# Performance work log

Measured on AMD Instinct MI355X. Metric: run time of the kernel, lower is better.

Reference implementation:

```python
import jax, jax.numpy as jnp
import numpy as np

N_EMBD = 1024
HEAD_SIZE = 64
B, T = 4, 4096


def setup_inputs() -> dict:
    key = jax.random.key(0)
    kx, kq, kk, kv = jax.random.split(key, 4)
    x = jax.random.normal(kx, (B, T, N_EMBD), dtype=jnp.float32)
    Wq = jax.random.normal(kq, (N_EMBD, HEAD_SIZE), dtype=jnp.float32) * (N_EMBD ** -0.5)
    Wk = jax.random.normal(kk, (N_EMBD, HEAD_SIZE), dtype=jnp.float32) * (N_EMBD ** -0.5)
    Wv = jax.random.normal(kv, (N_EMBD, HEAD_SIZE), dtype=jnp.float32) * (N_EMBD ** -0.5)
    return {"x": x, "Wq": Wq, "Wk": Wk, "Wv": Wv}


def reference(x, Wq, Wk, Wv):
    # x: [B, T, C]; projections: [B, T, H]
    Bv, Tv, C = x.shape
    q = jnp.einsum('btc,ch->bth', x, Wq)
    k = jnp.einsum('btc,ch->bth', x, Wk)
    v = jnp.einsum('btc,ch->bth', x, Wv)
    # NOTE: original scales by C**-0.5 where C = n_embd (not head_size)
    scale = C ** -0.5
    wei = jnp.einsum('bth,bsh->bts', q, k) * scale  # [B, T, T]
    causal = jnp.tril(jnp.ones((Tv, Tv), dtype=bool))
    wei = jnp.where(causal[None, :, :], wei, -jnp.inf)
    wei = jax.nn.softmax(wei, axis=-1)
    # dropout p=0.0 (eval) -> identity
    out = jnp.einsum('bts,bsh->bth', wei, v)  # [B, T, H]
    return out
```

## Files before the change

### kernel.cpp

```cpp
#include <hip/hip_runtime.h>
#include <math.h>

#define Tt 4096
#define Cc 1024
#define Hh 64

typedef __attribute__((ext_vector_type(8))) short bf16x8;
typedef __attribute__((ext_vector_type(4))) float f32x4;
typedef unsigned int u32;

__device__ inline unsigned short f2bf(float f) {
    unsigned u = __float_as_uint(f);
    u = (u + 0x7FFFu + ((u >> 16) & 1u)) >> 16;
    return (unsigned short)u;
}

__global__ __launch_bounds__(256) void wt_build(
    const float* __restrict__ Wq, const float* __restrict__ Wk,
    const float* __restrict__ Wv, unsigned short* __restrict__ Wt)
{
    int e = blockIdx.x * 256 + threadIdx.x;
    int k = e & 1023, n = e >> 10;
    float v;
    if (n < 64)       v = Wq[k * 64 + n] * 0.03125f;
    else if (n < 128) v = Wk[k * 64 + (n - 64)];
    else              v = Wv[k * 64 + (n - 128)];
    Wt[n * 1024 + k] = f2bf(v);
}

__global__ __launch_bounds__(256, 2) void qkv_gemm(
    const float* __restrict__ x, const unsigned short* __restrict__ wt,
    unsigned short* __restrict__ qb, unsigned short* __restrict__ kb,
    unsigned short* __restrict__ vt)
{
    __shared__ unsigned short as_[32 * 1024];

    const int t = threadIdx.x, w = t >> 6, lane = t & 63;
    const int col = lane & 15, quad = lane >> 4;
    const int m0 = blockIdx.x * 32;

    {
        const float* xr = x + (long)m0 * Cc;
#pragma unroll
        for (int i = 0; i < 32; ++i) {
            float4 v = *(const float4*)&xr[i * Cc + t * 4];
            ushort4 pk = { f2bf(v.x), f2bf(v.y), f2bf(v.z), f2bf(v.w) };
            int woff = (t * 4) ^ ((i & 7) << 3);
            *(ushort4*)&as_[i * 1024 + woff] = pk;
        }
    }
    __syncthreads();

    const unsigned short* aB[2];
#pragma unroll
    for (int kc = 0; kc < 2; ++kc)
        aB[kc] = &as_[col * 1024 + ((kc * 32 + quad * 8) ^ ((col & 7) << 3))];

    const unsigned short* pB[3];
#pragma unroll
    for (int nt = 0; nt < 3; ++nt)
        pB[nt] = wt + ((w * 3 + nt) * 16 + col) * 1024 + quad * 8;

    f32x4 acc[2][3];
#pragma unroll
    for (int mt = 0; mt < 2; ++mt)
#pragma unroll
        for (int nt = 0; nt < 3; ++nt) acc[mt][nt] = (f32x4){0.f, 0.f, 0.f, 0.f};

    bf16x8 bfr[2][3][2];
    bf16x8 afr[2][2][2];

#pragma unroll
    for (int nt = 0; nt < 3; ++nt)
#pragma unroll
        for (int kc = 0; kc < 2; ++kc)
            bfr[0][nt][kc] = *(const bf16x8*)(pB[nt] + kc * 32);
#pragma unroll
    for (int mt = 0; mt < 2; ++mt)
#pragma unroll
        for (int kc = 0; kc < 2; ++kc)
            afr[0][mt][kc] = *(const bf16x8*)(aB[kc] + mt * 16 * 1024);

#pragma unroll
    for (int k = 0; k < 16; ++k) {
        const int cur = k & 1, nxt = cur ^ 1;
        if (k < 15) {
            const int ko = (k + 1) * 64;
#pragma unroll
            for (int nt = 0; nt < 3; ++nt)
#pragma unroll
                for (int kc = 0; kc < 2; ++kc)
                    bfr[nxt][nt][kc] = *(const bf16x8*)(pB[nt] + ko + kc * 32);
#pragma unroll
            for (int mt = 0; mt < 2; ++mt)
#pragma unroll
                for (int kc = 0; kc < 2; ++kc)
                    afr[nxt][mt][kc] = *(const bf16x8*)(aB[kc] + mt * 16 * 1024 + ko);
        }
#pragma unroll
        for (int kc = 0; kc < 2; ++kc)
#pragma unroll
            for (int nt = 0; nt < 3; ++nt)
#pragma unroll
                for (int mt = 0; mt < 2; ++mt)
                    acc[mt][nt] = __builtin_amdgcn_mfma_f32_16x16x32_bf16(
                        afr[cur][mt][kc], bfr[cur][nt][kc], acc[mt][nt], 0, 0, 0);
    }

    const long bidx = m0 >> 12;
    const int tbase = m0 & 4095;
#pragma unroll
    for (int mt = 0; mt < 2; ++mt)
#pragma unroll
        for (int nt = 0; nt < 3; ++nt) {
            int ntg = w * 3 + nt;
            int n = ntg * 16 + col;
            int row = m0 + mt * 16 + quad * 4;
            if (ntg < 4) {
#pragma unroll
                for (int reg = 0; reg < 4; ++reg)
                    qb[(long)(row + reg) * Hh + n] = f2bf(acc[mt][nt][reg]);
            } else if (ntg < 8) {
#pragma unroll
                for (int reg = 0; reg < 4; ++reg)
                    kb[(long)(row + reg) * Hh + (n - 64)] = f2bf(acc[mt][nt][reg]);
            } else {
                int h = n - 128;
                ushort4 pk = { f2bf(acc[mt][nt][0]), f2bf(acc[mt][nt][1]),
                               f2bf(acc[mt][nt][2]), f2bf(acc[mt][nt][3]) };
                *(ushort4*)&vt[(bidx * Hh + h) * (long)Tt + tbase + mt * 16 + quad * 4] = pk;
            }
        }
}

#define LDP 56
#define LDO 68

__global__ __launch_bounds__(256) void attn(
    const unsigned short* __restrict__ qg, const unsigned short* __restrict__ kg,
    const unsigned short* __restrict__ vtg,
    float* __restrict__ po, float* __restrict__ pls)
{
    __shared__ __align__(16) char smem[49664];
    float* o_red       = (float*)smem;
    float* lred        = (float*)(smem + 34816);
    unsigned short* pl = (unsigned short*)(smem + 35328);

    const int p    = blockIdx.x;
    const int qt   = 127 - (p >> 3);
    const int b    = p & 3;
    const int half = (p >> 2) & 1;
    const int tid  = (b << 7) | qt;
    const long qrow0 = (long)b * Tt + qt * 32;
    const int nkt = qt + 1;
    const int n0  = (nkt + 1) >> 1;
    const int cnt = half ? (nkt - n0) : n0;
    const int ust = half ? n0 : 0;

    const int t = threadIdx.x, w = t >> 6, lane = t & 63;
    const int col = lane & 15, quad = lane >> 4;
    const int plbase = w * 32 * LDP;

    bf16x8 qf[2][2];
#pragma unroll
    for (int mt = 0; mt < 2; ++mt)
#pragma unroll
        for (int kc = 0; kc < 2; ++kc)
            qf[mt][kc] = *(const bf16x8*)&qg[(qrow0 + mt * 16 + col) * Hh + kc * 32 + quad * 8];

    f32x4 oacc[2][4];
#pragma unroll
    for (int mt = 0; mt < 2; ++mt)
#pragma unroll
        for (int nt = 0; nt < 4; ++nt) oacc[mt][nt] = (f32x4){0.f, 0.f, 0.f, 0.f};
    float lsum[2][4] = {{0.f,0.f,0.f,0.f},{0.f,0.f,0.f,0.f}};

    for (int iu = w; iu < cnt; iu += 4) {
        const int u = ust + iu;
        const long krow0 = (long)b * Tt + u * 32;
        bf16x8 kf[2][2];
#pragma unroll
        for (int nt = 0; nt < 2; ++nt)
#pragma unroll
            for (int kc = 0; kc < 2; ++kc)
                kf[nt][kc] = *(const bf16x8*)&kg[(krow0 + nt * 16 + col) * Hh + kc * 32 + quad * 8];
        f32x4 s[2][2];
#pragma unroll
        for (int mt = 0; mt < 2; ++mt)
#pragma unroll
            for (int nt = 0; nt < 2; ++nt) {
                s[mt][nt] = (f32x4){0.f, 0.f, 0.f, 0.f};
#pragma unroll
                for (int kc = 0; kc < 2; ++kc)
                    s[mt][nt] = __builtin_amdgcn_mfma_f32_16x16x32_bf16(qf[mt][kc], kf[nt][kc], s[mt][nt], 0, 0, 0);
            }
#pragma unroll
        for (int mt = 0; mt < 2; ++mt)
#pragma unroll
            for (int reg = 0; reg < 4; ++reg) {
                int rloc = mt * 16 + quad * 4 + reg;
                if (u == qt) {
                    if (col > rloc)      s[mt][0][reg] = -INFINITY;
                    if (16 + col > rloc) s[mt][1][reg] = -INFINITY;
                }
                float p0 = __expf(s[mt][0][reg]);
                float p1 = __expf(s[mt][1][reg]);
                lsum[mt][reg] += p0 + p1;
                pl[plbase + rloc * LDP + col]      = f2bf(p0);
                pl[plbase + rloc * LDP + 16 + col] = f2bf(p1);
            }
        bf16x8 af0 = *(const bf16x8*)&pl[plbase + col * LDP + quad * 8];
        bf16x8 af1 = *(const bf16x8*)&pl[plbase + (16 + col) * LDP + quad * 8];
#pragma unroll
        for (int nt = 0; nt < 4; ++nt) {
            bf16x8 vf = *(const bf16x8*)&vtg[((long)b * Hh + nt * 16 + col) * Tt + u * 32 + quad * 8];
            oacc[0][nt] = __builtin_amdgcn_mfma_f32_16x16x32_bf16(af0, vf, oacc[0][nt], 0, 0, 0);
            oacc[1][nt] = __builtin_amdgcn_mfma_f32_16x16x32_bf16(af1, vf, oacc[1][nt], 0, 0, 0);
        }
    }

#pragma unroll
    for (int mt = 0; mt < 2; ++mt)
#pragma unroll
        for (int reg = 0; reg < 4; ++reg) {
            float l = lsum[mt][reg];
            l += __shfl_xor(l, 1); l += __shfl_xor(l, 2);
            l += __shfl_xor(l, 4); l += __shfl_xor(l, 8);
            if (col == 0) lred[w * 32 + mt * 16 + quad * 4 + reg] = l;
        }
#pragma unroll
    for (int mt = 0; mt < 2; ++mt)
#pragma unroll
        for (int nt = 0; nt < 4; ++nt)
#pragma unroll
            for (int reg = 0; reg < 4; ++reg)
                o_red[(w * 32 + mt * 16 + quad * 4 + reg) * LDO + nt * 16 + col] = oacc[mt][nt][reg];
    __syncthreads();
    if (t < 32)
        pls[(tid * 2 + half) * 32 + t] = lred[t] + lred[32 + t] + lred[64 + t] + lred[96 + t];
    float* pob = po + ((long)tid * 2 + half) * 2048;
#pragma unroll
    for (int j = 0; j < 8; ++j) {
        int e = t + 256 * j, r = e >> 6, c = e & 63;
        pob[e] = o_red[r * LDO + c] + o_red[(32 + r) * LDO + c]
               + o_red[(64 + r) * LDO + c] + o_red[(96 + r) * LDO + c];
    }
}

__global__ __launch_bounds__(256) void combine(
    const float* __restrict__ po, const float* __restrict__ pls, float* __restrict__ out)
{
    const int g = blockIdx.x;
    const long orow = (((long)(g >> 7)) * Tt + (long)(g & 127) * 32) * Hh;
    const float* p0 = po + (long)g * 2 * 2048;
    const float* p1 = p0 + 2048;
    const float* l0 = pls + g * 2 * 32;
    const float* l1 = l0 + 32;
    const int t = threadIdx.x;
#pragma unroll
    for (int j = 0; j < 8; ++j) {
        int e = t + 256 * j, r = e >> 6;
        out[orow + e] = (p0[e] + p1[e]) / (l0[r] + l1[r]);
    }
}

extern "C" void kernel_launch(void* const* d_in, const int* in_sizes, int n_in,
                              void* d_out, int out_size, void* d_ws, size_t ws_size,
                              hipStream_t stream)
{
    const float* x  = (const float*)d_in[0];
    const float* Wq = (const float*)d_in[1];
    const float* Wk = (const float*)d_in[2];
    const float* Wv = (const float*)d_in[3];
    float* outp = (float*)d_out;

    unsigned short* wt = (unsigned short*)d_ws;
    unsigned short* qb = wt + 196608;
    unsigned short* kb = qb + 1048576;
    unsigned short* vt = kb + 1048576;
    float* po  = (float*)(vt + 1048576);
    float* pls = po + 2097152;

    wt_build<<<dim3(768), dim3(256), 0, stream>>>(Wq, Wk, Wv, wt);
    qkv_gemm<<<dim3(512), dim3(256), 0, stream>>>(x, wt, qb, kb, vt);
    attn<<<dim3(1024), dim3(256), 0, stream>>>(qb, kb, vt, po, pls);
    combine<<<dim3(512), dim3(256), 0, stream>>>(po, pls, outp);
}
```

Measured before the change: 160.4 us.

## Pre-cast x to bf16 and stage GEMM tile via direct global-to-LDS loads

Adds a separate kernel that converts x from fp32 to bf16 in workspace. The QKV GEMM then fills its LDS tile with global_load_lds directly, keeping the same XOR swizzle. The attention kernel also aliases its P staging buffer onto the O-reduction buffer, which shrinks LDS use and may raise occupancy. The cost is an extra launch and an extra full read/write pass over x, plus a risk of a race from the aliased LDS if the reuse phases overlap.

```diff
diff --git a/kernel.cpp b/kernel.cpp
--- a/kernel.cpp
+++ b/kernel.cpp
@@ -13,6 +13,24 @@
     unsigned u = __float_as_uint(f);
     u = (u + 0x7FFFu + ((u >> 16) & 1u)) >> 16;
     return (unsigned short)u;
+}
+
+__device__ inline void gl_lds16(const unsigned short* g, unsigned short* l) {
+    __builtin_amdgcn_global_load_lds(
+        (const __attribute__((address_space(1))) u32*)g,
+        (__attribute__((address_space(3))) u32*)l, 16, 0, 0);
+}
+
+__global__ __launch_bounds__(256) void xcast(
+    const float* __restrict__ x, unsigned short* __restrict__ xb)
+{
+    const long i = ((long)blockIdx.x * 256 + threadIdx.x) * 8;
+    float4 a = *(const float4*)&x[i];
+    float4 b = *(const float4*)&x[i + 4];
+    ushort4 lo = { f2bf(a.x), f2bf(a.y), f2bf(a.z), f2bf(a.w) };
+    ushort4 hi = { f2bf(b.x), f2bf(b.y), f2bf(b.z), f2bf(b.w) };
+    *(ushort4*)&xb[i]     = lo;
+    *(ushort4*)&xb[i + 4] = hi;
 }
 
 __global__ __launch_bounds__(256) void wt_build(
@@ -29,7 +47,7 @@
 }
 
 __global__ __launch_bounds__(256, 2) void qkv_gemm(
-    const float* __restrict__ x, const unsigned short* __restrict__ wt,
+    const unsigned short* __restrict__ xbf, const unsigned short* __restrict__ wt,
     unsigned short* __restrict__ qb, unsigned short* __restrict__ kb,
     unsigned short* __restrict__ vt)
 {
@@ -40,13 +58,14 @@
     const int m0 = blockIdx.x * 32;
 
     {
-        const float* xr = x + (long)m0 * Cc;
-#pragma unroll
-        for (int i = 0; i < 32; ++i) {
-            float4 v = *(const float4*)&xr[i * Cc + t * 4];
-            ushort4 pk = { f2bf(v.x), f2bf(v.y), f2bf(v.z), f2bf(v.w) };
-            int woff = (t * 4) ^ ((i & 7) << 3);
-            *(ushort4*)&as_[i * 1024 + woff] = pk;
+        const int rh = t >> 7;
+        const int s  = t & 127;
+        const unsigned short* src = xbf + (long)m0 * 1024;
+#pragma unroll
+        for (int j = 0; j < 16; ++j) {
+            int r = 2 * j + rh;
+            gl_lds16(src + r * 1024 + (s ^ (r & 7)) * 8,
+                     as_ + j * 2048 + w * 512);
         }
     }
     __syncthreads();
@@ -141,10 +160,10 @@
     const unsigned short* __restrict__ vtg,
     float* __restrict__ po, float* __restrict__ pls)
 {
-    __shared__ __align__(16) char smem[49664];
+    __shared__ __align__(16) char smem[35328];
     float* o_red       = (float*)smem;
     float* lred        = (float*)(smem + 34816);
-    unsigned short* pl = (unsigned short*)(smem + 35328);
+    unsigned short* pl = (unsigned short*)smem;
 
     const int p    = blockIdx.x;
     const int qt   = 127 - (p >> 3);
@@ -159,7 +178,7 @@
 
     const int t = threadIdx.x, w = t >> 6, lane = t & 63;
     const int col = lane & 15, quad = lane >> 4;
-    const int plbase = w * 32 * LDP;
+    const int plbase = w * 4352;
 
     bf16x8 qf[2][2];
 #pragma unroll
@@ -280,9 +299,11 @@
     unsigned short* vt = kb + 1048576;
     float* po  = (float*)(vt + 1048576);
     float* pls = po + 2097152;
-
-    wt_build<<<dim3(768), dim3(256), 0, stream>>>(Wq, Wk, Wv, wt);
-    qkv_gemm<<<dim3(512), dim3(256), 0, stream>>>(x, wt, qb, kb, vt);
-    attn<<<dim3(1024), dim3(256), 0, stream>>>(qb, kb, vt, po, pls);
-    combine<<<dim3(512), dim3(256), 0, stream>>>(po, pls, outp);
-}
+    unsigned short* xbf = (unsigned short*)(pls + 32768);
+
+    xcast   <<<dim3(8192), dim3(256), 0, stream>>>(x, xbf);
+    wt_build<<<dim3(768),  dim3(256), 0, stream>>>(Wq, Wk, Wv, wt);
+    qkv_gemm<<<dim3(512),  dim3(256), 0, stream>>>(xbf, wt, qb, kb, vt);
+    attn    <<<dim3(1024), dim3(256), 0, stream>>>(qb, kb, vt, po, pls);
+    combine <<<dim3(512),  dim3(256), 0, stream>>>(po, pls, outp);
+}
```

Result: slower. 171.4 us (+6.9%).

## Double-buffer K/V register loads in attention loop and batch x loads in QKV GEMM

Applied to the files above, without the earlier changes.

The attention loop now prefetches the next K and V fragments into a second register set while computing the current tile, so global-load latency overlaps with MFMA work. It also raises wave priority around the MFMA blocks. Shared memory is shrunk by aliasing the P scratch buffer onto the output-reduction area. The QKV GEMM staging issues 16 float4 loads before converting and storing them, to get more memory-level parallelism. These changes cost more registers, and the aliasing relies on P use being finished before o_red is written.

```diff
diff --git a/kernel.cpp b/kernel.cpp
--- a/kernel.cpp
+++ b/kernel.cpp
@@ -40,13 +40,23 @@
     const int m0 = blockIdx.x * 32;
 
     {
-        const float* xr = x + (long)m0 * Cc;
-#pragma unroll
-        for (int i = 0; i < 32; ++i) {
-            float4 v = *(const float4*)&xr[i * Cc + t * 4];
-            ushort4 pk = { f2bf(v.x), f2bf(v.y), f2bf(v.z), f2bf(v.w) };
-            int woff = (t * 4) ^ ((i & 7) << 3);
-            *(ushort4*)&as_[i * 1024 + woff] = pk;
+        const float* xb = x + (long)m0 * Cc;
+        float4 vbuf[16];
+#pragma unroll
+        for (int g = 0; g < 2; ++g) {
+#pragma unroll
+            for (int s = 0; s < 16; ++s) {
+                int row = g * 16 + s;
+                vbuf[s] = *(const float4*)&xb[row * 1024 + t * 4];
+            }
+#pragma unroll
+            for (int s = 0; s < 16; ++s) {
+                int row = g * 16 + s;
+                ushort4 pk = { f2bf(vbuf[s].x), f2bf(vbuf[s].y),
+                               f2bf(vbuf[s].z), f2bf(vbuf[s].w) };
+                int woff = (t * 4) ^ ((row & 7) << 3);
+                *(ushort4*)&as_[row * 1024 + woff] = pk;
+            }
         }
     }
     __syncthreads();
@@ -141,10 +151,10 @@
     const unsigned short* __restrict__ vtg,
     float* __restrict__ po, float* __restrict__ pls)
 {
-    __shared__ __align__(16) char smem[49664];
+    __shared__ __align__(16) char smem[35328];
     float* o_red       = (float*)smem;
     float* lred        = (float*)(smem + 34816);
-    unsigned short* pl = (unsigned short*)(smem + 35328);
+    unsigned short* pl = (unsigned short*)smem;
 
     const int p    = blockIdx.x;
     const int qt   = 127 - (p >> 3);
@@ -159,7 +169,7 @@
 
     const int t = threadIdx.x, w = t >> 6, lane = t & 63;
     const int col = lane & 15, quad = lane >> 4;
-    const int plbase = w * 32 * LDP;
+    const int plbase = w * 4352;
 
     bf16x8 qf[2][2];
 #pragma unroll
@@ -175,16 +185,23 @@
         for (int nt = 0; nt < 4; ++nt) oacc[mt][nt] = (f32x4){0.f, 0.f, 0.f, 0.f};
     float lsum[2][4] = {{0.f,0.f,0.f,0.f},{0.f,0.f,0.f,0.f}};
 
-    for (int iu = w; iu < cnt; iu += 4) {
-        const int u = ust + iu;
-        const long krow0 = (long)b * Tt + u * 32;
-        bf16x8 kf[2][2];
+    auto loadK = [&](bf16x8 (&kf)[2][2], int iu_) {
+        const long krow0 = (long)b * Tt + (ust + iu_) * 32;
 #pragma unroll
         for (int nt = 0; nt < 2; ++nt)
 #pragma unroll
             for (int kc = 0; kc < 2; ++kc)
                 kf[nt][kc] = *(const bf16x8*)&kg[(krow0 + nt * 16 + col) * Hh + kc * 32 + quad * 8];
+    };
+    auto loadV = [&](bf16x8 (&vf)[4], int iu_) {
+        const int u = ust + iu_;
+#pragma unroll
+        for (int nt = 0; nt < 4; ++nt)
+            vf[nt] = *(const bf16x8*)&vtg[((long)b * Hh + nt * 16 + col) * Tt + u * 32 + quad * 8];
+    };
+    auto compute = [&](bf16x8 (&kf)[2][2], bf16x8 (&vf)[4], int u) {
         f32x4 s[2][2];
+        __builtin_amdgcn_s_setprio(1);
 #pragma unroll
         for (int mt = 0; mt < 2; ++mt)
 #pragma unroll
@@ -192,8 +209,10 @@
                 s[mt][nt] = (f32x4){0.f, 0.f, 0.f, 0.f};
 #pragma unroll
                 for (int kc = 0; kc < 2; ++kc)
-                    s[mt][nt] = __builtin_amdgcn_mfma_f32_16x16x32_bf16(qf[mt][kc], kf[nt][kc], s[mt][nt], 0, 0, 0);
-            }
+                    s[mt][nt] = __builtin_amdgcn_mfma_f32_16x16x32_bf16(
+                        qf[mt][kc], kf[nt][kc], s[mt][nt], 0, 0, 0);
+            }
+        __builtin_amdgcn_s_setprio(0);
 #pragma unroll
         for (int mt = 0; mt < 2; ++mt)
 #pragma unroll
@@ -211,12 +230,27 @@
             }
         bf16x8 af0 = *(const bf16x8*)&pl[plbase + col * LDP + quad * 8];
         bf16x8 af1 = *(const bf16x8*)&pl[plbase + (16 + col) * LDP + quad * 8];
+        __builtin_amdgcn_s_setprio(1);
 #pragma unroll
         for (int nt = 0; nt < 4; ++nt) {
-            bf16x8 vf = *(const bf16x8*)&vtg[((long)b * Hh + nt * 16 + col) * Tt + u * 32 + quad * 8];
-            oacc[0][nt] = __builtin_amdgcn_mfma_f32_16x16x32_bf16(af0, vf, oacc[0][nt], 0, 0, 0);
-            oacc[1][nt] = __builtin_amdgcn_mfma_f32_16x16x32_bf16(af1, vf, oacc[1][nt], 0, 0, 0);
-        }
+            oacc[0][nt] = __builtin_amdgcn_mfma_f32_16x16x32_bf16(af0, vf[nt], oacc[0][nt], 0, 0, 0);
+            oacc[1][nt] = __builtin_amdgcn_mfma_f32_16x16x32_bf16(af1, vf[nt], oacc[1][nt], 0, 0, 0);
+        }
+        __builtin_amdgcn_s_setprio(0);
+    };
+
+    bf16x8 kA[2][2], vA[4], kB[2][2], vB[4];
+    int iu = w;
+    if (iu < cnt) { loadK(kA, iu); loadV(vA, iu); }
+    while (iu < cnt) {
+        int i1 = iu + 4;
+        if (i1 < cnt) { loadK(kB, i1); loadV(vB, i1); }
+        compute(kA, vA, ust + iu);
+        if (i1 >= cnt) break;
+        int i2 = i1 + 4;
+        if (i2 < cnt) { loadK(kA, i2); loadV(vA, i2); }
+        compute(kB, vB, ust + i1);
+        iu = i2;
     }
 
 #pragma unroll
```

New measurement: 161.4 us. No clear change (+0.6%).
